# Kernel optimization log

Measured on AMD Instinct MI355X. Metric: run time of the kernel, lower is better.

## Reference

```python
import jax, jax.numpy as jnp
import numpy as np

DIM = 256
HEAD_DIM = 32
HEADS = DIM // HEAD_DIM
SCALE = HEAD_DIM ** -0.5


def setup_inputs() -> dict:
    key = jax.random.key(0)
    ks = jax.random.split(key, 5)
    B, C, H, W = 2, DIM, 48, 48
    x = jax.random.normal(ks[0], (B, C, H, W), jnp.float32)
    # qkv 1x1 conv weight [3C, C] (no bias, qkv_bias=False)
    w_qkv = jax.random.normal(ks[1], (3 * C, C), jnp.float32) * (C ** -0.5)
    # depthwise 3x3 conv (groups=C): weight [C, 1, 3, 3] + bias [C]
    w_lepe = jax.random.normal(ks[2], (C, 1, 3, 3), jnp.float32) * (1.0 / 3.0)
    b_lepe = jax.random.normal(ks[3], (C,), jnp.float32) * 0.01
    # proj 1x1 conv weight [C, C] + bias [C]
    w_proj = jax.random.normal(ks[4], (C, C), jnp.float32) * (C ** -0.5)
    b_proj = jnp.zeros((C,), jnp.float32)
    return {"x": x, "w_qkv": w_qkv, "w_lepe": w_lepe, "b_lepe": b_lepe,
            "w_proj": w_proj, "b_proj": b_proj}


def reference(x, w_qkv, w_lepe, b_lepe, w_proj, b_proj):
    B, C, H, W = x.shape
    N = H * W
    h, d = HEADS, HEAD_DIM
    # qkv 1x1 conv -> [B, 3C, H, W], reshape to [B, h, 3d, N], chunk on dim 2
    qkv = jnp.einsum('oc,bchw->bohw', w_qkv, x).reshape(B, h, 3 * d, N)
    q, k, v = jnp.split(qkv, 3, axis=2)  # each [B, h, d, N]
    # lepe: depthwise 3x3 conv on v reshaped back to [B, C, H, W]
    v4 = v.reshape(B, C, H, W)
    lepe = jax.lax.conv_general_dilated(
        v4, w_lepe, window_strides=(1, 1), padding='SAME',
        dimension_numbers=('NCHW', 'OIHW', 'NCHW'),
        feature_group_count=C) + b_lepe[None, :, None, None]
    # attn = k^T @ q * scale, softmax over the KEY dim (dim=-2)
    attn = jax.nn.softmax(jnp.einsum('bhdk,bhdq->bhkq', k, q) * SCALE, axis=-2)
    # out = v @ attn -> [B, h, d, N] -> [B, C, H, W]
    out = jnp.einsum('bhdk,bhkq->bhdq', v, attn).reshape(B, C, H, W)
    out = out + lepe
    # proj 1x1 conv + bias (dropouts are identity at p=0)
    out = jnp.einsum('oc,bchw->bohw', w_proj, out) + b_proj[None, :, None, None]
    return out
```

## Files before the change

### kernel.cpp

```cpp
#include <hip/hip_runtime.h>
#include <hip/hip_bf16.h>

typedef __bf16 bf16;
typedef __bf16 bf16x8 __attribute__((ext_vector_type(8)));
typedef __bf16 bf16x4 __attribute__((ext_vector_type(4)));
typedef float  f32x4  __attribute__((ext_vector_type(4)));
typedef float  f32x2  __attribute__((ext_vector_type(2)));

#define NB    2
#define CCH   256
#define NPIX  2304
#define WIMG  48
#define SLOG2E 0.25503487f
#define NSPLIT 4
#define KSEG   576
#define TK     64
#define NITER  9

__global__ __launch_bounds__(256) void qkv_gemm(const float* __restrict__ x,
                                                const float* __restrict__ w,
                                                bf16* __restrict__ Qt,
                                                bf16* __restrict__ Kt,
                                                bf16* __restrict__ Vb) {
    __shared__ __align__(16) bf16 xT[64][40];
    const int tid  = threadIdx.x;
    const int lane = tid & 63;
    const int wv   = tid >> 6;
    const int wn   = wv & 1, wo = wv >> 1;
    const int l15  = lane & 15, l4 = lane >> 4;
    const int g0 = blockIdx.x * 64;
    const int b  = g0 / NPIX;
    const int n0 = g0 % NPIX;
    const int o0 = blockIdx.y * 64;
    const float* xb = x + (size_t)b * CCH * NPIX;

    f32x4 acc[2][2] = {};

    for (int kc = 0; kc < 8; ++kc) {
        const int c0 = kc * 32;
        for (int r = 0; r < 8; ++r) {
            int idx = r * 256 + tid;
            int c = idx >> 6, n = idx & 63;
            xT[n][c] = (bf16)xb[(size_t)(c0 + c) * NPIX + n0 + n];
        }
        __syncthreads();
        bf16x8 afr[2], bfr[2];
        for (int at = 0; at < 2; ++at) {
            const float* wp = w + (size_t)(o0 + wo * 32 + at * 16 + l15) * CCH + c0 + l4 * 8;
            f32x4 w0 = *(const f32x4*)wp;
            f32x4 w1 = *(const f32x4*)(wp + 4);
            bf16x8 a;
            for (int i = 0; i < 4; ++i) { a[i] = (bf16)w0[i]; a[i + 4] = (bf16)w1[i]; }
            afr[at] = a;
        }
        for (int bt = 0; bt < 2; ++bt)
            bfr[bt] = *(const bf16x8*)&xT[wn * 32 + bt * 16 + l15][l4 * 8];
        for (int at = 0; at < 2; ++at)
            for (int bt = 0; bt < 2; ++bt)
                acc[at][bt] = __builtin_amdgcn_mfma_f32_16x16x32_bf16(afr[at], bfr[bt],
                                                                     acc[at][bt], 0, 0, 0);
        __syncthreads();
    }

    for (int at = 0; at < 2; ++at) {
        const int otile = o0 + wo * 32 + at * 16;
        const int h    = otile / 96;
        const int role = (otile % 96) / 32;
        const int ddb  = (otile % 32) + l4 * 4;
        const int bh   = b * 8 + h;
        for (int bt = 0; bt < 2; ++bt) {
            const int n = n0 + wn * 32 + bt * 16 + l15;
            if (role == 2) {
                for (int r = 0; r < 4; ++r)
                    Vb[(size_t)(bh * 32 + ddb + r) * NPIX + n] = (bf16)acc[at][bt][r];
            } else if (role == 1) {
                bf16x4 pk;
                for (int r = 0; r < 4; ++r) pk[r] = (bf16)(acc[at][bt][r] * SLOG2E);
                *(bf16x4*)&Kt[((size_t)bh * NPIX + n) * 32 + ddb] = pk;
            } else {
                bf16x4 pk;
                for (int r = 0; r < 4; ++r) pk[r] = (bf16)acc[at][bt][r];
                *(bf16x4*)&Qt[((size_t)bh * NPIX + n) * 32 + ddb] = pk;
            }
        }
    }
}

__global__ __launch_bounds__(256, 4) void attn_kernel(const bf16* __restrict__ Qt,
                                                      const bf16* __restrict__ Kt,
                                                      const bf16* __restrict__ Vb,
                                                      float* __restrict__ Opart,
                                                      float* __restrict__ MLpart) {
    __shared__ __align__(16) bf16 Ktile[64][40];
    __shared__ __align__(16) bf16 Vtile[32][72];
    __shared__ __align__(16) bf16 Ptile[64][72];
    const int tid  = threadIdx.x;
    const int lane = tid & 63;
    const int wv   = tid >> 6;
    const int l15  = lane & 15, l4 = lane >> 4;
    const int bh    = blockIdx.y;
    const int split = blockIdx.z;
    const int q0 = blockIdx.x * 64;
    const int q  = q0 + wv * 16 + l15;

    const bf16* Kbh = Kt + (size_t)bh * NPIX * 32 + (size_t)split * KSEG * 32;
    const bf16* Vbh = Vb + (size_t)bh * 32 * NPIX + split * KSEG;

    bf16x8 qf = *(const bf16x8*)&Qt[((size_t)bh * NPIX + q) * 32 + l4 * 8];

    const int krow = tid >> 2, kcol = (tid & 3) * 8;
    const int vd   = tid >> 3, vc   = (tid & 7) * 8;
    const bf16* ksrc = Kbh + (size_t)krow * 32 + kcol;
    const bf16* vsrc = Vbh + (size_t)vd * NPIX + vc;

    bf16x8 ka, va;
    ka = *(const bf16x8*)(ksrc);
    va = *(const bf16x8*)(vsrc);
    *(bf16x8*)&Ktile[krow][kcol] = ka;
    *(bf16x8*)&Vtile[vd][vc]     = va;
    __syncthreads();

    f32x4 O0 = {}, O1 = {};
    float m_run = -INFINITY, l_run = 0.f;
    const int qrow = wv * 16 + l15;

    for (int kt = 0; kt < NITER; ++kt) {
        if (kt + 1 < NITER) {
            ka = *(const bf16x8*)(ksrc + (size_t)(kt + 1) * TK * 32);
            va = *(const bf16x8*)(vsrc + (kt + 1) * TK);
        }

        f32x4 s[4];
        for (int rt = 0; rt < 4; ++rt) {
            bf16x8 a = *(const bf16x8*)&Ktile[rt * 16 + l15][l4 * 8];
            f32x4 z = {};
            s[rt] = __builtin_amdgcn_mfma_f32_16x16x32_bf16(a, qf, z, 0, 0, 0);
        }

        float tmax = -INFINITY;
        for (int rt = 0; rt < 4; ++rt)
            for (int r = 0; r < 4; ++r) tmax = fmaxf(tmax, s[rt][r]);
        tmax = fmaxf(tmax, __shfl_xor(tmax, 16));
        tmax = fmaxf(tmax, __shfl_xor(tmax, 32));
        const float m_new = fmaxf(m_run, tmax);
        const float f = __builtin_amdgcn_exp2f(m_run - m_new);
        float psum = 0.f;
        for (int rt = 0; rt < 4; ++rt) {
            bf16x4 pk;
            for (int r = 0; r < 4; ++r) {
                float p = __builtin_amdgcn_exp2f(s[rt][r] - m_new);
                psum += p;
                pk[r] = (bf16)p;
            }
            *(bf16x4*)&Ptile[qrow][rt * 16 + l4 * 4] = pk;
        }
        psum += __shfl_xor(psum, 16);
        psum += __shfl_xor(psum, 32);
        l_run = l_run * f + psum;
        m_run = m_new;
        for (int i = 0; i < 4; ++i) { O0[i] *= f; O1[i] *= f; }

        for (int ks = 0; ks < 2; ++ks) {
            bf16x8 pb = *(const bf16x8*)&Ptile[qrow][ks * 32 + l4 * 8];
            bf16x8 v0 = *(const bf16x8*)&Vtile[l15][ks * 32 + l4 * 8];
            bf16x8 v1 = *(const bf16x8*)&Vtile[16 + l15][ks * 32 + l4 * 8];
            O0 = __builtin_amdgcn_mfma_f32_16x16x32_bf16(v0, pb, O0, 0, 0, 0);
            O1 = __builtin_amdgcn_mfma_f32_16x16x32_bf16(v1, pb, O1, 0, 0, 0);
        }
        __syncthreads();
        if (kt + 1 < NITER) {
            *(bf16x8*)&Ktile[krow][kcol] = ka;
            *(bf16x8*)&Vtile[vd][vc]     = va;
        }
        __syncthreads();
    }

    f32x4* Op4 = (f32x4*)(Opart + ((size_t)(split * 16 + bh) * NPIX + q) * 32);
    Op4[l4]     = O0;
    Op4[4 + l4] = O1;
    if (l4 == 0) {
        f32x2 ml; ml[0] = m_run; ml[1] = l_run;
        *(f32x2*)&MLpart[((size_t)(split * 16 + bh) * NPIX + q) * 2] = ml;
    }
}

__global__ __launch_bounds__(256) void epilogue_kernel(const float* __restrict__ Opart,
                                                       const float* __restrict__ MLpart,
                                                       const bf16* __restrict__ Vb,
                                                       const float* __restrict__ wl,
                                                       const float* __restrict__ bl,
                                                       bf16* __restrict__ aout) {
    __shared__ float wnorm[NSPLIT][72];
    __shared__ float vals[32][69];
    const int tid = threadIdx.x;
    const int bh  = blockIdx.y;
    const int q0  = blockIdx.x * 64;

    if (tid < 64) {
        const int q = q0 + tid;
        float mv[NSPLIT], lv[NSPLIT], m = -INFINITY;
        for (int s = 0; s < NSPLIT; ++s) {
            f32x2 ml = *(const f32x2*)&MLpart[((size_t)(s * 16 + bh) * NPIX + q) * 2];
            mv[s] = ml[0]; lv[s] = ml[1];
            m = fmaxf(m, ml[0]);
        }
        float wsv[NSPLIT], denom = 0.f;
        for (int s = 0; s < NSPLIT; ++s) {
            wsv[s] = __builtin_amdgcn_exp2f(mv[s] - m);
            denom += wsv[s] * lv[s];
        }
        const float inv = 1.f / denom;
        for (int s = 0; s < NSPLIT; ++s) wnorm[s][tid] = wsv[s] * inv;
    }
    __syncthreads();

    {
        const int d  = tid & 31;
        const int qg = tid >> 5;
        for (int j = 0; j < 8; ++j) {
            const int qq = qg * 8 + j;
            const int q  = q0 + qq;
            float v = 0.f;
            for (int s = 0; s < NSPLIT; ++s)
                v += wnorm[s][qq] * Opart[((size_t)(s * 16 + bh) * NPIX + q) * 32 + d];
            vals[d][qq] = v;
        }
    }
    __syncthreads();

    const int d2 = tid >> 3;
    const int n8 = (tid & 7) * 8;
    const int c  = bh * 32 + d2;
    const int ch = c & 255;
    const float bias = bl[ch];
    float wgt[9];
    for (int i = 0; i < 9; ++i) wgt[i] = wl[ch * 9 + i];
    const bf16* vrow = Vb + (size_t)c * NPIX;

    for (int j = 0; j < 8; ++j) {
        const int q = q0 + n8 + j;
        float val = vals[d2][n8 + j];
        const int y = q / WIMG, xx = q % WIMG;
        float acc = bias;
        for (int dy = -1; dy <= 1; ++dy) {
            const int yy = y + dy;
            if (yy < 0 || yy >= WIMG) continue;
            for (int dx = -1; dx <= 1; ++dx) {
                const int xc = xx + dx;
                if (xc < 0 || xc >= WIMG) continue;
                acc += (float)vrow[yy * WIMG + xc] * wgt[(dy + 1) * 3 + dx + 1];
            }
        }
        aout[(size_t)c * NPIX + q] = (bf16)(val + acc);
    }
}

__global__ __launch_bounds__(256) void proj_gemm(const bf16* __restrict__ ain,
                                                 const float* __restrict__ w,
                                                 const float* __restrict__ bp,
                                                 float* __restrict__ out) {
    __shared__ __align__(16) bf16 aT[64][40];
    const int tid  = threadIdx.x;
    const int lane = tid & 63;
    const int wv   = tid >> 6;
    const int wn   = wv & 1, wo = wv >> 1;
    const int l15  = lane & 15, l4 = lane >> 4;
    const int g0 = blockIdx.x * 64;
    const int b  = g0 / NPIX;
    const int n0 = g0 % NPIX;
    const int o0 = blockIdx.y * 64;
    const bf16* ab = ain + (size_t)b * CCH * NPIX;

    f32x4 acc[2][2] = {};
    for (int kc = 0; kc < 8; ++kc) {
        const int c0 = kc * 32;
        for (int r = 0; r < 8; ++r) {
            int idx = r * 256 + tid;
            int ci = idx >> 6, n = idx & 63;
            aT[n][ci] = ab[(size_t)(c0 + ci) * NPIX + n0 + n];
        }
        __syncthreads();
        bf16x8 afr[2], bfr[2];
        for (int at = 0; at < 2; ++at) {
            const float* wp = w + (size_t)(o0 + wo * 32 + at * 16 + l15) * CCH + c0 + l4 * 8;
            f32x4 w0 = *(const f32x4*)wp;
            f32x4 w1 = *(const f32x4*)(wp + 4);
            bf16x8 a;
            for (int i = 0; i < 4; ++i) { a[i] = (bf16)w0[i]; a[i + 4] = (bf16)w1[i]; }
            afr[at] = a;
        }
        for (int bt = 0; bt < 2; ++bt)
            bfr[bt] = *(const bf16x8*)&aT[wn * 32 + bt * 16 + l15][l4 * 8];
        for (int at = 0; at < 2; ++at)
            for (int bt = 0; bt < 2; ++bt)
                acc[at][bt] = __builtin_amdgcn_mfma_f32_16x16x32_bf16(afr[at], bfr[bt],
                                                                     acc[at][bt], 0, 0, 0);
        __syncthreads();
    }
    for (int at = 0; at < 2; ++at)
        for (int bt = 0; bt < 2; ++bt) {
            const int n = n0 + wn * 32 + bt * 16 + l15;
            for (int r = 0; r < 4; ++r) {
                const int o = o0 + wo * 32 + at * 16 + l4 * 4 + r;
                out[(size_t)(b * 256 + o) * NPIX + n] = acc[at][bt][r] + bp[o];
            }
        }
}

extern "C" void kernel_launch(void* const* d_in, const int* in_sizes, int n_in,
                              void* d_out, int out_size, void* d_ws, size_t ws_size,
                              hipStream_t stream) {
    const float* x      = (const float*)d_in[0];
    const float* w_qkv  = (const float*)d_in[1];
    const float* w_lepe = (const float*)d_in[2];
    const float* b_lepe = (const float*)d_in[3];
    const float* w_proj = (const float*)d_in[4];
    const float* b_proj = (const float*)d_in[5];
    float* out = (float*)d_out;

    bf16* Qt   = (bf16*)d_ws;
    bf16* Kt   = Qt + 1179648;
    bf16* Vb   = Kt + 1179648;
    bf16* aout = Vb + 1179648;
    float* Opart  = (float*)((char*)d_ws + 9437184);
    float* MLpart = Opart + 4718592;

    qkv_gemm      <<<dim3(72, 12),    256, 0, stream>>>(x, w_qkv, Qt, Kt, Vb);
    attn_kernel   <<<dim3(36, 16, 4), 256, 0, stream>>>(Qt, Kt, Vb, Opart, MLpart);
    epilogue_kernel<<<dim3(36, 16),   256, 0, stream>>>(Opart, MLpart, Vb, w_lepe, b_lepe, aout);
    proj_gemm     <<<dim3(72, 4),     256, 0, stream>>>(aout, w_proj, b_proj, out);
}
```

Measured before the change: 164.7 us.

## Stage full activation tile in LDS once with vectorized loads in QKV and proj GEMMs

Both 1x1-conv GEMM kernels now load the whole 64-pixel by 256-channel activation tile into LDS up front, instead of staging 32 channels per k-step. The loads use 16-byte vector reads and pack channel pairs into 32-bit LDS writes. This removes the per-iteration barriers and the scalar, strided transposing loads. The cost is a much larger LDS footprint per block (about 33 KB), which may reduce occupancy, and there is no overlap of loading with MFMA work.

```diff
diff --git a/kernel.cpp b/kernel.cpp
--- a/kernel.cpp
+++ b/kernel.cpp
@@ -4,6 +4,8 @@
 typedef __bf16 bf16;
 typedef __bf16 bf16x8 __attribute__((ext_vector_type(8)));
 typedef __bf16 bf16x4 __attribute__((ext_vector_type(4)));
+typedef __bf16 bf16x2 __attribute__((ext_vector_type(2)));
+typedef unsigned short ushort8 __attribute__((ext_vector_type(8)));
 typedef float  f32x4  __attribute__((ext_vector_type(4)));
 typedef float  f32x2  __attribute__((ext_vector_type(2)));
 
@@ -22,7 +24,7 @@
                                                 bf16* __restrict__ Qt,
                                                 bf16* __restrict__ Kt,
                                                 bf16* __restrict__ Vb) {
-    __shared__ __align__(16) bf16 xT[64][40];
+    __shared__ __align__(16) bf16 xT[64][264];
     const int tid  = threadIdx.x;
     const int lane = tid & 63;
     const int wv   = tid >> 6;
@@ -34,19 +36,26 @@
     const int o0 = blockIdx.y * 64;
     const float* xb = x + (size_t)b * CCH * NPIX;
 
+    {
+        const int nq  = (tid & 15) * 4;
+        const int cp0 = tid >> 4;
+        for (int i = 0; i < 8; ++i) {
+            const int c = (i * 16 + cp0) * 2;
+            f32x4 a0 = *(const f32x4*)&xb[(size_t)c * NPIX + n0 + nq];
+            f32x4 a1 = *(const f32x4*)&xb[(size_t)(c + 1) * NPIX + n0 + nq];
+            for (int j = 0; j < 4; ++j) {
+                bf16x2 p; p[0] = (bf16)a0[j]; p[1] = (bf16)a1[j];
+                *(bf16x2*)&xT[nq + j][c] = p;
+            }
+        }
+    }
+    __syncthreads();
+
     f32x4 acc[2][2] = {};
-
     for (int kc = 0; kc < 8; ++kc) {
-        const int c0 = kc * 32;
-        for (int r = 0; r < 8; ++r) {
-            int idx = r * 256 + tid;
-            int c = idx >> 6, n = idx & 63;
-            xT[n][c] = (bf16)xb[(size_t)(c0 + c) * NPIX + n0 + n];
-        }
-        __syncthreads();
         bf16x8 afr[2], bfr[2];
         for (int at = 0; at < 2; ++at) {
-            const float* wp = w + (size_t)(o0 + wo * 32 + at * 16 + l15) * CCH + c0 + l4 * 8;
+            const float* wp = w + (size_t)(o0 + wo * 32 + at * 16 + l15) * CCH + kc * 32 + l4 * 8;
             f32x4 w0 = *(const f32x4*)wp;
             f32x4 w1 = *(const f32x4*)(wp + 4);
             bf16x8 a;
@@ -54,12 +63,11 @@
             afr[at] = a;
         }
         for (int bt = 0; bt < 2; ++bt)
-            bfr[bt] = *(const bf16x8*)&xT[wn * 32 + bt * 16 + l15][l4 * 8];
+            bfr[bt] = *(const bf16x8*)&xT[wn * 32 + bt * 16 + l15][kc * 32 + l4 * 8];
         for (int at = 0; at < 2; ++at)
             for (int bt = 0; bt < 2; ++bt)
                 acc[at][bt] = __builtin_amdgcn_mfma_f32_16x16x32_bf16(afr[at], bfr[bt],
                                                                      acc[at][bt], 0, 0, 0);
-        __syncthreads();
     }
 
     for (int at = 0; at < 2; ++at) {
@@ -259,7 +267,7 @@
                                                  const float* __restrict__ w,
                                                  const float* __restrict__ bp,
                                                  float* __restrict__ out) {
-    __shared__ __align__(16) bf16 aT[64][40];
+    __shared__ __align__(16) bf16 aT[64][264];
     const int tid  = threadIdx.x;
     const int lane = tid & 63;
     const int wv   = tid >> 6;
@@ -271,18 +279,26 @@
     const int o0 = blockIdx.y * 64;
     const bf16* ab = ain + (size_t)b * CCH * NPIX;
 
+    {
+        const int nq  = (tid & 7) * 8;
+        const int cp0 = tid >> 3;
+        for (int i = 0; i < 4; ++i) {
+            const int c = (i * 32 + cp0) * 2;
+            ushort8 a0 = *(const ushort8*)&ab[(size_t)c * NPIX + n0 + nq];
+            ushort8 a1 = *(const ushort8*)&ab[(size_t)(c + 1) * NPIX + n0 + nq];
+            for (int j = 0; j < 8; ++j) {
+                unsigned int u = (unsigned int)a0[j] | ((unsigned int)a1[j] << 16);
+                *(unsigned int*)&aT[nq + j][c] = u;
+            }
+        }
+    }
+    __syncthreads();
+
     f32x4 acc[2][2] = {};
     for (int kc = 0; kc < 8; ++kc) {
-        const int c0 = kc * 32;
-        for (int r = 0; r < 8; ++r) {
-            int idx = r * 256 + tid;
-            int ci = idx >> 6, n = idx & 63;
-            aT[n][ci] = ab[(size_t)(c0 + ci) * NPIX + n0 + n];
-        }
-        __syncthreads();
         bf16x8 afr[2], bfr[2];
         for (int at = 0; at < 2; ++at) {
-            const float* wp = w + (size_t)(o0 + wo * 32 + at * 16 + l15) * CCH + c0 + l4 * 8;
+            const float* wp = w + (size_t)(o0 + wo * 32 + at * 16 + l15) * CCH + kc * 32 + l4 * 8;
             f32x4 w0 = *(const f32x4*)wp;
             f32x4 w1 = *(const f32x4*)(wp + 4);
             bf16x8 a;
@@ -290,12 +306,11 @@
             afr[at] = a;
         }
         for (int bt = 0; bt < 2; ++bt)
-            bfr[bt] = *(const bf16x8*)&aT[wn * 32 + bt * 16 + l15][l4 * 8];
+            bfr[bt] = *(const bf16x8*)&aT[wn * 32 + bt * 16 + l15][kc * 32 + l4 * 8];
         for (int at = 0; at < 2; ++at)
             for (int bt = 0; bt < 2; ++bt)
                 acc[at][bt] = __builtin_amdgcn_mfma_f32_16x16x32_bf16(afr[at], bfr[bt],
                                                                      acc[at][bt], 0, 0, 0);
-        __syncthreads();
     }
     for (int at = 0; at < 2; ++at)
         for (int bt = 0; bt < 2; ++bt) {
```

Result: faster. 145.2 us (-11.9%).
